# Kernel optimization log

Measured on AMD Instinct MI355X. Metric: run time of the kernel, lower is better.

Reference implementation:

```python
import jax, jax.numpy as jnp
import numpy as np

EPS = 1e-8

def setup_inputs() -> dict:
    key = jax.random.key(0)
    k1, = jax.random.split(key, 1)
    B, C, T = 16, 256, 16000
    inp = jax.random.normal(k1, (B, C, T), dtype=jnp.float32)
    gain = jnp.ones((1, C, 1), dtype=jnp.float32)
    bias = jnp.zeros((1, C, 1), dtype=jnp.float32)
    return {"input": inp, "gain": gain, "bias": bias}

def reference(input, gain, bias):
    # input: [B, C, T]
    B, C, T = input.shape
    step_sum = input.sum(axis=1)            # [B, T]
    step_pow_sum = (input * input).sum(axis=1)  # [B, T]
    cum_sum = jnp.cumsum(step_sum, axis=1)      # [B, T]
    cum_pow_sum = jnp.cumsum(step_pow_sum, axis=1)
    # entry count: C, 2C, ..., T*C
    entry_cnt = (jnp.arange(1, T + 1, dtype=input.dtype) * C)[None, :]  # [1, T]
    cum_mean = cum_sum / entry_cnt
    cum_var = (cum_pow_sum - 2.0 * cum_mean * cum_sum) / entry_cnt + cum_mean * cum_mean
    cum_std = jnp.sqrt(cum_var + EPS)
    x = (input - cum_mean[:, None, :]) / cum_std[:, None, :]
    return x * gain + bias
```

## Files before the change

### kernel.cpp

```cpp
#include <hip/hip_runtime.h>

constexpr int B = 16;
constexpr int C = 256;
constexpr int T = 16000;
constexpr int Q = T / 4;
constexpr float EPS = 1e-8f;
constexpr int CG  = 4;
constexpr int CPG = C / CG;
constexpr int CPB = 8;
constexpr int RUN = 16;

typedef float f4 __attribute__((ext_vector_type(4)));

__global__ __launch_bounds__(256) void step_sums_kernel(
    const float* __restrict__ x,
    float* __restrict__ ssum_part,
    float* __restrict__ spow_part) {
  const int b  = blockIdx.z;
  const int g  = blockIdx.y;
  const int t4 = blockIdx.x * blockDim.x + threadIdx.x;
  if (t4 >= Q) return;

  const f4* xb = reinterpret_cast<const f4*>(x + ((size_t)b * C + (size_t)g * CPG) * T);
  f4 s = {0.f, 0.f, 0.f, 0.f};
  f4 p = {0.f, 0.f, 0.f, 0.f};

#pragma unroll 8
  for (int c = 0; c < CPG; ++c) {
    f4 v = __builtin_nontemporal_load(&xb[(size_t)c * Q + t4]);
    s += v;
    p += v * v;
  }
  reinterpret_cast<f4*>(ssum_part + ((size_t)g * B + b) * T)[t4] = s;
  reinterpret_cast<f4*>(spow_part + ((size_t)g * B + b) * T)[t4] = p;
}

__global__ __launch_bounds__(256) void scan_kernel(
    const float* __restrict__ ssum_part,
    const float* __restrict__ spow_part,
    float* __restrict__ mean_out,
    float* __restrict__ istd_out) {
  const int b   = blockIdx.x;
  const int j   = threadIdx.x;
  const int lane = j & 63;
  const int wid  = j >> 6;
  const bool active = (j * RUN) < Q;

  f4 S[RUN], P[RUN];
#pragma unroll
  for (int k = 0; k < RUN; ++k) { S[k] = (f4){0,0,0,0}; P[k] = (f4){0,0,0,0}; }

  if (active) {
#pragma unroll
    for (int g = 0; g < CG; ++g) {
      const f4* sp = reinterpret_cast<const f4*>(ssum_part + ((size_t)g * B + b) * T);
      const f4* pp = reinterpret_cast<const f4*>(spow_part + ((size_t)g * B + b) * T);
#pragma unroll
      for (int k = 0; k < RUN; ++k) {
        S[k] += sp[j * RUN + k];
        P[k] += pp[j * RUN + k];
      }
    }
  }

  float rs = 0.f, rp = 0.f;
#pragma unroll
  for (int k = 0; k < RUN; ++k) {
#pragma unroll
    for (int c = 0; c < 4; ++c) {
      rs += S[k][c]; S[k][c] = rs;
      rp += P[k][c]; P[k][c] = rp;
    }
  }

  const double ts = (double)rs, tp = (double)rp;
  double cs = ts, cp = tp;
#pragma unroll
  for (int off = 1; off < 64; off <<= 1) {
    double ns = __shfl_up(cs, off);
    double np = __shfl_up(cp, off);
    if (lane >= off) { cs += ns; cp += np; }
  }
  __shared__ double wss[4], wsp[4];
  if (lane == 63) { wss[wid] = cs; wsp[wid] = cp; }
  __syncthreads();

  double pre_s = cs - ts;
  double pre_p = cp - tp;
#pragma unroll
  for (int w = 0; w < 4; ++w) {
    if (w < wid) { pre_s += wss[w]; pre_p += wsp[w]; }
  }

  if (active) {
    f4* mo = reinterpret_cast<f4*>(mean_out + (size_t)b * T);
    f4* io = reinterpret_cast<f4*>(istd_out + (size_t)b * T);
#pragma unroll
    for (int k = 0; k < RUN; ++k) {
      f4 m, iv;
#pragma unroll
      for (int c = 0; c < 4; ++c) {
        const int i = (j * RUN + k) * 4 + c;
        const float cnt = (float)(i + 1) * (float)C;
        const float cum_s = (float)(pre_s + (double)S[k][c]);
        const float cum_p = (float)(pre_p + (double)P[k][c]);
        const float mean  = cum_s / cnt;
        const float var   = cum_p / cnt - mean * mean;
        m[c]  = mean;
        iv[c] = rsqrtf(var + EPS);
      }
      mo[j * RUN + k] = m;
      io[j * RUN + k] = iv;
    }
  }
}

__global__ __launch_bounds__(256) void apply_kernel(
    const float* __restrict__ x,
    const float* __restrict__ mean,
    const float* __restrict__ istd,
    const float* __restrict__ gain,
    const float* __restrict__ bias,
    float* __restrict__ out) {
  const int b  = blockIdx.z;
  const int c0 = blockIdx.y * CPB;
  const int t4 = blockIdx.x * blockDim.x + threadIdx.x;
  if (t4 >= Q) return;

  const f4 m  = reinterpret_cast<const f4*>(mean + (size_t)b * T)[t4];
  const f4 is = reinterpret_cast<const f4*>(istd + (size_t)b * T)[t4];

  const f4* xb = reinterpret_cast<const f4*>(x   + ((size_t)b * C + c0) * T);
  f4*       ob = reinterpret_cast<f4*>      (out + ((size_t)b * C + c0) * T);

#pragma unroll
  for (int i = 0; i < CPB; ++i) {
    const float g  = gain[c0 + i];
    const float bi = bias[c0 + i];
    f4 v = __builtin_nontemporal_load(&xb[(size_t)i * Q + t4]);
    f4 o = (v - m) * is * g + bi;
    __builtin_nontemporal_store(o, &ob[(size_t)i * Q + t4]);
  }
}

extern "C" void kernel_launch(void* const* d_in, const int* in_sizes, int n_in,
                              void* d_out, int out_size, void* d_ws, size_t ws_size,
                              hipStream_t stream) {
  const float* x    = (const float*)d_in[0];
  const float* gain = (const float*)d_in[1];
  const float* bias = (const float*)d_in[2];
  float* out = (float*)d_out;

  float* ssum_part = (float*)d_ws;
  float* spow_part = ssum_part + (size_t)CG * B * T;
  float* mean      = spow_part + (size_t)CG * B * T;
  float* istd      = mean      + (size_t)B * T;

  dim3 g1((Q + 255) / 256, CG, B);
  step_sums_kernel<<<g1, 256, 0, stream>>>(x, ssum_part, spow_part);

  scan_kernel<<<B, 256, 0, stream>>>(ssum_part, spow_part, mean, istd);

  dim3 g3((Q + 255) / 256, C / CPB, B);
  apply_kernel<<<g3, 256, 0, stream>>>(x, mean, istd, gain, bias, out);
}
```

Baseline: 469.8 us.

## Fuse channel sums with per-segment scan and fold cross-segment prefix into apply

The three-kernel pipeline becomes two. The first kernel sums each batch over channels and runs a local prefix scan inside a 64-float4 segment, writing segment scans and per-segment totals in double. The apply kernel reduces the preceding segment totals with wave shuffles, computes mean and inverse std inline, then normalizes. This removes the low-parallelism 16-block scan kernel and the mean/istd round trip through memory. In exchange, both kernels use a coarser grid of about 1008 blocks with long per-thread channel loops, and the x loads are no longer nontemporal.

```diff
diff --git a/kernel.cpp b/kernel.cpp
--- a/kernel.cpp
+++ b/kernel.cpp
@@ -4,142 +4,127 @@
 constexpr int C = 256;
 constexpr int T = 16000;
 constexpr int Q = T / 4;
+constexpr int SEG = 64;
+constexpr int NSEG = (Q + SEG - 1) / SEG;
 constexpr float EPS = 1e-8f;
-constexpr int CG  = 4;
-constexpr int CPG = C / CG;
-constexpr int CPB = 8;
-constexpr int RUN = 16;
 
 typedef float f4 __attribute__((ext_vector_type(4)));
 
-__global__ __launch_bounds__(256) void step_sums_kernel(
+__global__ __launch_bounds__(256) void sumscan_kernel(
     const float* __restrict__ x,
-    float* __restrict__ ssum_part,
-    float* __restrict__ spow_part) {
-  const int b  = blockIdx.z;
-  const int g  = blockIdx.y;
-  const int t4 = blockIdx.x * blockDim.x + threadIdx.x;
-  if (t4 >= Q) return;
+    float* __restrict__ scan_s,
+    float* __restrict__ scan_p,
+    double* __restrict__ tot_s,
+    double* __restrict__ tot_p) {
+  const int seg = blockIdx.x;
+  const int b   = blockIdx.y;
+  const int w   = threadIdx.x >> 6;
+  const int l   = threadIdx.x & 63;
+  const int t4  = seg * SEG + l;
+  const bool act = t4 < Q;
 
-  const f4* xb = reinterpret_cast<const f4*>(x + ((size_t)b * C + (size_t)g * CPG) * T);
   f4 s = {0.f, 0.f, 0.f, 0.f};
   f4 p = {0.f, 0.f, 0.f, 0.f};
-
+  if (act) {
+    const f4* xb = reinterpret_cast<const f4*>(x + (size_t)b * C * T);
 #pragma unroll 8
-  for (int c = 0; c < CPG; ++c) {
-    f4 v = __builtin_nontemporal_load(&xb[(size_t)c * Q + t4]);
-    s += v;
-    p += v * v;
-  }
-  reinterpret_cast<f4*>(ssum_part + ((size_t)g * B + b) * T)[t4] = s;
-  reinterpret_cast<f4*>(spow_part + ((size_t)g * B + b) * T)[t4] = p;
-}
-
-__global__ __launch_bounds__(256) void scan_kernel(
-    const float* __restrict__ ssum_part,
-    const float* __restrict__ spow_part,
-    float* __restrict__ mean_out,
-    float* __restrict__ istd_out) {
-  const int b   = blockIdx.x;
-  const int j   = threadIdx.x;
-  const int lane = j & 63;
-  const int wid  = j >> 6;
-  const bool active = (j * RUN) < Q;
-
-  f4 S[RUN], P[RUN];
-#pragma unroll
-  for (int k = 0; k < RUN; ++k) { S[k] = (f4){0,0,0,0}; P[k] = (f4){0,0,0,0}; }
-
-  if (active) {
-#pragma unroll
-    for (int g = 0; g < CG; ++g) {
-      const f4* sp = reinterpret_cast<const f4*>(ssum_part + ((size_t)g * B + b) * T);
-      const f4* pp = reinterpret_cast<const f4*>(spow_part + ((size_t)g * B + b) * T);
-#pragma unroll
-      for (int k = 0; k < RUN; ++k) {
-        S[k] += sp[j * RUN + k];
-        P[k] += pp[j * RUN + k];
-      }
+    for (int cc = 0; cc < C / 4; ++cc) {
+      const int c = cc * 4 + w;
+      f4 v = xb[(size_t)c * Q + t4];
+      s += v;
+      p += v * v;
     }
   }
 
-  float rs = 0.f, rp = 0.f;
-#pragma unroll
-  for (int k = 0; k < RUN; ++k) {
-#pragma unroll
-    for (int c = 0; c < 4; ++c) {
-      rs += S[k][c]; S[k][c] = rs;
-      rp += P[k][c]; P[k][c] = rp;
-    }
-  }
+  __shared__ f4 ls[4][64], lp[4][64];
+  ls[w][l] = s;
+  lp[w][l] = p;
+  __syncthreads();
 
-  const double ts = (double)rs, tp = (double)rp;
-  double cs = ts, cp = tp;
+  if (w != 0) return;
+
+  f4 cs = ls[0][l] + ls[1][l] + ls[2][l] + ls[3][l];
+  f4 cp = lp[0][l] + lp[1][l] + lp[2][l] + lp[3][l];
+  cs[1] += cs[0]; cs[2] += cs[1]; cs[3] += cs[2];
+  cp[1] += cp[0]; cp[2] += cp[1]; cp[3] += cp[2];
+
+  double rs = (double)cs[3], rp = (double)cp[3];
 #pragma unroll
   for (int off = 1; off < 64; off <<= 1) {
-    double ns = __shfl_up(cs, off);
-    double np = __shfl_up(cp, off);
-    if (lane >= off) { cs += ns; cp += np; }
+    double ns = __shfl_up(rs, off);
+    double np = __shfl_up(rp, off);
+    if (l >= off) { rs += ns; rp += np; }
   }
-  __shared__ double wss[4], wsp[4];
-  if (lane == 63) { wss[wid] = cs; wsp[wid] = cp; }
-  __syncthreads();
+  const double es = rs - (double)cs[3];
+  const double ep = rp - (double)cp[3];
 
-  double pre_s = cs - ts;
-  double pre_p = cp - tp;
+  if (act) {
+    f4 os, op;
 #pragma unroll
-  for (int w = 0; w < 4; ++w) {
-    if (w < wid) { pre_s += wss[w]; pre_p += wsp[w]; }
+    for (int i = 0; i < 4; ++i) {
+      os[i] = (float)(es + (double)cs[i]);
+      op[i] = (float)(ep + (double)cp[i]);
+    }
+    reinterpret_cast<f4*>(scan_s + (size_t)b * T)[t4] = os;
+    reinterpret_cast<f4*>(scan_p + (size_t)b * T)[t4] = op;
   }
-
-  if (active) {
-    f4* mo = reinterpret_cast<f4*>(mean_out + (size_t)b * T);
-    f4* io = reinterpret_cast<f4*>(istd_out + (size_t)b * T);
-#pragma unroll
-    for (int k = 0; k < RUN; ++k) {
-      f4 m, iv;
-#pragma unroll
-      for (int c = 0; c < 4; ++c) {
-        const int i = (j * RUN + k) * 4 + c;
-        const float cnt = (float)(i + 1) * (float)C;
-        const float cum_s = (float)(pre_s + (double)S[k][c]);
-        const float cum_p = (float)(pre_p + (double)P[k][c]);
-        const float mean  = cum_s / cnt;
-        const float var   = cum_p / cnt - mean * mean;
-        m[c]  = mean;
-        iv[c] = rsqrtf(var + EPS);
-      }
-      mo[j * RUN + k] = m;
-      io[j * RUN + k] = iv;
-    }
+  if (l == 63) {
+    tot_s[b * NSEG + seg] = rs;
+    tot_p[b * NSEG + seg] = rp;
   }
 }
 
 __global__ __launch_bounds__(256) void apply_kernel(
     const float* __restrict__ x,
-    const float* __restrict__ mean,
-    const float* __restrict__ istd,
+    const float* __restrict__ scan_s,
+    const float* __restrict__ scan_p,
+    const double* __restrict__ tot_s,
+    const double* __restrict__ tot_p,
     const float* __restrict__ gain,
     const float* __restrict__ bias,
     float* __restrict__ out) {
-  const int b  = blockIdx.z;
-  const int c0 = blockIdx.y * CPB;
-  const int t4 = blockIdx.x * blockDim.x + threadIdx.x;
-  if (t4 >= Q) return;
+  const int seg = blockIdx.x;
+  const int b   = blockIdx.y;
+  const int w   = threadIdx.x >> 6;
+  const int l   = threadIdx.x & 63;
+  const int t4  = seg * SEG + l;
+  const bool act = t4 < Q;
 
-  const f4 m  = reinterpret_cast<const f4*>(mean + (size_t)b * T)[t4];
-  const f4 is = reinterpret_cast<const f4*>(istd + (size_t)b * T)[t4];
+  double vs = (l < seg) ? tot_s[b * NSEG + l] : 0.0;
+  double vp = (l < seg) ? tot_p[b * NSEG + l] : 0.0;
+#pragma unroll
+  for (int off = 32; off > 0; off >>= 1) {
+    vs += __shfl_xor(vs, off);
+    vp += __shfl_xor(vp, off);
+  }
 
-  const f4* xb = reinterpret_cast<const f4*>(x   + ((size_t)b * C + c0) * T);
-  f4*       ob = reinterpret_cast<f4*>      (out + ((size_t)b * C + c0) * T);
+  if (act) {
+    const f4 cs = reinterpret_cast<const f4*>(scan_s + (size_t)b * T)[t4];
+    const f4 cp = reinterpret_cast<const f4*>(scan_p + (size_t)b * T)[t4];
+    f4 m, is;
+#pragma unroll
+    for (int i = 0; i < 4; ++i) {
+      const int t = t4 * 4 + i;
+      const float cnt  = (float)(t + 1) * (float)C;
+      const float cums = (float)(vs + (double)cs[i]);
+      const float cump = (float)(vp + (double)cp[i]);
+      const float mean = cums / cnt;
+      const float var  = cump / cnt - mean * mean;
+      m[i]  = mean;
+      is[i] = rsqrtf(var + EPS);
+    }
 
-#pragma unroll
-  for (int i = 0; i < CPB; ++i) {
-    const float g  = gain[c0 + i];
-    const float bi = bias[c0 + i];
-    f4 v = __builtin_nontemporal_load(&xb[(size_t)i * Q + t4]);
-    f4 o = (v - m) * is * g + bi;
-    __builtin_nontemporal_store(o, &ob[(size_t)i * Q + t4]);
+    const f4* xb = reinterpret_cast<const f4*>(x   + (size_t)b * C * T);
+    f4*       ob = reinterpret_cast<f4*>      (out + (size_t)b * C * T);
+#pragma unroll 8
+    for (int cc = 0; cc < C / 4; ++cc) {
+      const int c = cc * 4 + w;
+      const float g  = gain[c];
+      const float bi = bias[c];
+      f4 v = xb[(size_t)c * Q + t4];
+      f4 o = (v - m) * is * g + bi;
+      __builtin_nontemporal_store(o, &ob[(size_t)c * Q + t4]);
+    }
   }
 }
 
@@ -151,16 +136,13 @@
   const float* bias = (const float*)d_in[2];
   float* out = (float*)d_out;
 
-  float* ssum_part = (float*)d_ws;
-  float* spow_part = ssum_part + (size_t)CG * B * T;
-  float* mean      = spow_part + (size_t)CG * B * T;
-  float* istd      = mean      + (size_t)B * T;
+  float*  scan_s = (float*)d_ws;
+  float*  scan_p = scan_s + (size_t)B * T;
+  double* tot_s  = (double*)(scan_p + (size_t)B * T);
+  double* tot_p  = tot_s + (size_t)B * NSEG;
 
-  dim3 g1((Q + 255) / 256, CG, B);
-  step_sums_kernel<<<g1, 256, 0, stream>>>(x, ssum_part, spow_part);
-
-  scan_kernel<<<B, 256, 0, stream>>>(ssum_part, spow_part, mean, istd);
-
-  dim3 g3((Q + 255) / 256, C / CPB, B);
-  apply_kernel<<<g3, 256, 0, stream>>>(x, mean, istd, gain, bias, out);
+  dim3 grid(NSEG, B);
+  sumscan_kernel<<<grid, 256, 0, stream>>>(x, scan_s, scan_p, tot_s, tot_p);
+  apply_kernel<<<grid, 256, 0, stream>>>(x, scan_s, scan_p, tot_s, tot_p,
+                                         gain, bias, out);
 }
```

Result: no change. 475.5 us (+1.2%).
